# Optimization experiments

Hardware: AMD Instinct MI355X
Metric: run time of the kernel (lower is better)

The kernel has to match this reference:

```python
import jax, jax.numpy as jnp
import numpy as np

B, N = 65536, 128  # batch of point clouds, points per cloud

def setup_inputs() -> dict:
    key = jax.random.key(0)
    k1, k2 = jax.random.split(key)
    x = jax.random.normal(k1, (B, N, 3), dtype=jnp.float32)
    y = jax.random.normal(k2, (B, N, 3), dtype=jnp.float32)
    return {"x": x, "y": y}

def reference(x, y):
    # zero-center both point clouds
    xc = x - x.mean(axis=-2, keepdims=True)
    yc = y - y.mean(axis=-2, keepdims=True)
    # batched 3x3 covariance: C[..., j, k] = sum_i xc[..., i, j] * yc[..., i, k]
    C = jnp.einsum('...ij,...ik->...jk', xc, yc)
    # torch.linalg.svd returns (U, S, Vh); original code names Vh as V and forms R = U @ Vh
    U, _, Vh = jnp.linalg.svd(C)
    R = jnp.einsum('...ij,...jk->...ik', U, Vh)
    x_aligned = jnp.einsum('...ij,...jk->...ik', xc, R)
    # mean square deviation over all batch, point, and coordinate dims
    return jnp.mean((x_aligned - yc) ** 2)
```

## Files before the change

### kernel.cpp

```cpp
#include <hip/hip_runtime.h>
#include <math.h>


#define NPTS 128

__device__ __forceinline__ float xsum(float v, int m) {
    return v + __shfl_xor(v, m);
}

__global__ __launch_bounds__(256, 1) void kabsch_kernel(
        const float* __restrict__ x, const float* __restrict__ y,
        float* __restrict__ out, float scale) {
    const int tid  = threadIdx.x;
    const int lane = tid & 63;
    const int wave = tid >> 6;
    const int g    = lane >> 3;
    const int sub  = lane & 7;
    const int b    = blockIdx.x * 32 + wave * 8 + g;

    const float4* xq = (const float4*)(x + (size_t)b * (NPTS * 3) + sub * 48);
    const float4* yq = (const float4*)(y + (size_t)b * (NPTS * 3) + sub * 48);

    float sx0=0.f,sx1=0.f,sx2=0.f, sy0=0.f,sy1=0.f,sy2=0.f;
    float qx=0.f, qy=0.f;
    float c00=0.f,c01=0.f,c02=0.f,c10=0.f,c11=0.f,c12=0.f,c20=0.f,c21=0.f,c22=0.f;

    #pragma unroll
    for (int h = 0; h < 2; ++h) {
        float4 xv0 = xq[6*h+0], xv1 = xq[6*h+1], xv2 = xq[6*h+2];
        float4 xv3 = xq[6*h+3], xv4 = xq[6*h+4], xv5 = xq[6*h+5];
        float4 yv0 = yq[6*h+0], yv1 = yq[6*h+1], yv2 = yq[6*h+2];
        float4 yv3 = yq[6*h+3], yv4 = yq[6*h+4], yv5 = yq[6*h+5];

        float fx[24], fy[24];
        fx[ 0]=xv0.x; fx[ 1]=xv0.y; fx[ 2]=xv0.z; fx[ 3]=xv0.w;
        fx[ 4]=xv1.x; fx[ 5]=xv1.y; fx[ 6]=xv1.z; fx[ 7]=xv1.w;
        fx[ 8]=xv2.x; fx[ 9]=xv2.y; fx[10]=xv2.z; fx[11]=xv2.w;
        fx[12]=xv3.x; fx[13]=xv3.y; fx[14]=xv3.z; fx[15]=xv3.w;
        fx[16]=xv4.x; fx[17]=xv4.y; fx[18]=xv4.z; fx[19]=xv4.w;
        fx[20]=xv5.x; fx[21]=xv5.y; fx[22]=xv5.z; fx[23]=xv5.w;
        fy[ 0]=yv0.x; fy[ 1]=yv0.y; fy[ 2]=yv0.z; fy[ 3]=yv0.w;
        fy[ 4]=yv1.x; fy[ 5]=yv1.y; fy[ 6]=yv1.z; fy[ 7]=yv1.w;
        fy[ 8]=yv2.x; fy[ 9]=yv2.y; fy[10]=yv2.z; fy[11]=yv2.w;
        fy[12]=yv3.x; fy[13]=yv3.y; fy[14]=yv3.z; fy[15]=yv3.w;
        fy[16]=yv4.x; fy[17]=yv4.y; fy[18]=yv4.z; fy[19]=yv4.w;
        fy[20]=yv5.x; fy[21]=yv5.y; fy[22]=yv5.z; fy[23]=yv5.w;

        #pragma unroll
        for (int p = 0; p < 8; ++p) {
            float px0=fx[3*p], px1=fx[3*p+1], px2=fx[3*p+2];
            float py0=fy[3*p], py1=fy[3*p+1], py2=fy[3*p+2];
            sx0+=px0; sx1+=px1; sx2+=px2;
            sy0+=py0; sy1+=py1; sy2+=py2;
            qx = fmaf(px0,px0,fmaf(px1,px1,fmaf(px2,px2,qx)));
            qy = fmaf(py0,py0,fmaf(py1,py1,fmaf(py2,py2,qy)));
            c00=fmaf(px0,py0,c00); c01=fmaf(px0,py1,c01); c02=fmaf(px0,py2,c02);
            c10=fmaf(px1,py0,c10); c11=fmaf(px1,py1,c11); c12=fmaf(px1,py2,c12);
            c20=fmaf(px2,py0,c20); c21=fmaf(px2,py1,c21); c22=fmaf(px2,py2,c22);
        }
    }

    #pragma unroll
    for (int m = 1; m <= 4; m <<= 1) {
        sx0=xsum(sx0,m); sx1=xsum(sx1,m); sx2=xsum(sx2,m);
        sy0=xsum(sy0,m); sy1=xsum(sy1,m); sy2=xsum(sy2,m);
        qx =xsum(qx ,m); qy =xsum(qy ,m);
        c00=xsum(c00,m); c01=xsum(c01,m); c02=xsum(c02,m);
        c10=xsum(c10,m); c11=xsum(c11,m); c12=xsum(c12,m);
        c20=xsum(c20,m); c21=xsum(c21,m); c22=xsum(c22,m);
    }

    const float invN = 1.0f / (float)NPTS;
    float C00 = c00 - sx0*sy0*invN, C01 = c01 - sx0*sy1*invN, C02 = c02 - sx0*sy2*invN;
    float C10 = c10 - sx1*sy0*invN, C11 = c11 - sx1*sy1*invN, C12 = c12 - sx1*sy2*invN;
    float C20 = c20 - sx2*sy0*invN, C21 = c21 - sx2*sy1*invN, C22 = c22 - sx2*sy2*invN;
    float Sx = qx - (sx0*sx0 + sx1*sx1 + sx2*sx2) * invN;
    float Sy = qy - (sy0*sy0 + sy1*sy1 + sy2*sy2) * invN;

    float a00 = C00*C00 + C10*C10 + C20*C20;
    float a01 = C00*C01 + C10*C11 + C20*C21;
    float a02 = C00*C02 + C10*C12 + C20*C22;
    float a11 = C01*C01 + C11*C11 + C21*C21;
    float a12 = C01*C02 + C11*C12 + C21*C22;
    float a22 = C02*C02 + C12*C12 + C22*C22;

    float q = (a00 + a11 + a22) * (1.0f / 3.0f);
    float b00 = a00 - q, b11 = a11 - q, b22 = a22 - q;
    float p2 = (b00*b00 + b11*b11 + b22*b22
                + 2.0f * (a01*a01 + a02*a02 + a12*a12)) * (1.0f / 6.0f);
    float p = sqrtf(fmaxf(p2, 0.0f));
    float detB = b00 * (b11*b22 - a12*a12)
               - a01 * (a01*b22 - a12*a02)
               + a02 * (a01*a12 - b11*a02);
    float p3 = p * p * p;
    float r = (p3 > 1e-30f) ? (0.5f * detB / p3) : 0.0f;
    r = fminf(1.0f, fmaxf(-1.0f, r));
    float phi = acosf(r) * (1.0f / 3.0f);
    float two_p = 2.0f * p;
    float l1 = q + two_p * cosf(phi);
    float l3 = q + two_p * cosf(phi + 2.0943951023931953f);
    float l2 = 3.0f * q - l1 - l3;
    float nuc = sqrtf(fmaxf(l1, 0.0f)) + sqrtf(fmaxf(l2, 0.0f)) + sqrtf(fmaxf(l3, 0.0f));

    float term = Sx + Sy - 2.0f * nuc;

    term += __shfl_xor(term, 8);
    term += __shfl_xor(term, 16);
    term += __shfl_xor(term, 32);

    __shared__ float wsum[4];
    if (lane == 0) wsum[wave] = term;
    __syncthreads();
    if (tid == 0) {
        float t = (wsum[0] + wsum[1] + wsum[2] + wsum[3]) * scale;
        atomicAdd(out, t);
    }
}

extern "C" void kernel_launch(void* const* d_in, const int* in_sizes, int n_in,
                              void* d_out, int out_size, void* d_ws, size_t ws_size,
                              hipStream_t stream) {
    const float* x = (const float*)d_in[0];
    const float* y = (const float*)d_in[1];
    float* out = (float*)d_out;

    const int B = in_sizes[0] / (NPTS * 3);
    const float scale = 1.0f / ((float)B * (float)NPTS * 3.0f);

    hipMemsetAsync(out, 0, sizeof(float), stream);
    const int blocks = B / 32;
    kabsch_kernel<<<blocks, 256, 0, stream>>>(x, y, out, scale);
}
```

Measured before the change: 258.7 us.

## Stage point clouds through LDS with coalesced direct global-to-LDS loads

Each block now copies its 16 batches of x and y into shared memory using fully coalesced float4 loads, issued as direct global-to-LDS transfers when that builtin is available. Each batch is then processed by 16 lanes instead of 8, and one extra shuffle stage is added to the reduction. The launch-bounds occupancy hint rises from 1 to 3 blocks per CU, and there are twice as many blocks. The goal is to replace the strided per-lane global reads with coalesced ones and get more memory parallelism, at the cost of a block-wide barrier, 48KB of LDS per block, and possible LDS bank conflicts on the 6-float4 stride reads.

```diff
diff --git a/kernel.cpp b/kernel.cpp
--- a/kernel.cpp
+++ b/kernel.cpp
@@ -3,65 +3,91 @@
 
 
 #define NPTS 128
+#define BPB 16
+#define F4B 96
 
 __device__ __forceinline__ float xsum(float v, int m) {
     return v + __shfl_xor(v, m);
 }
 
-__global__ __launch_bounds__(256, 1) void kabsch_kernel(
-        const float* __restrict__ x, const float* __restrict__ y,
+__global__ __launch_bounds__(256, 3) void kabsch_kernel(
+        const float4* __restrict__ x4, const float4* __restrict__ y4,
         float* __restrict__ out, float scale) {
+    __shared__ float4 smem[2 * BPB * F4B];
+
     const int tid  = threadIdx.x;
     const int lane = tid & 63;
     const int wave = tid >> 6;
-    const int g    = lane >> 3;
-    const int sub  = lane & 7;
-    const int b    = blockIdx.x * 32 + wave * 8 + g;
 
-    const float4* xq = (const float4*)(x + (size_t)b * (NPTS * 3) + sub * 48);
-    const float4* yq = (const float4*)(y + (size_t)b * (NPTS * 3) + sub * 48);
+    const size_t blockBase = (size_t)blockIdx.x * (BPB * F4B);
+
+    {
+        const int rpw = (BPB * F4B) / (64 * 4);
+        #pragma unroll
+        for (int j = 0; j < rpw; ++j) {
+            const int idx = (wave * rpw + j) * 64;
+#if defined(__has_builtin)
+#if __has_builtin(__builtin_amdgcn_global_load_lds)
+            __builtin_amdgcn_global_load_lds(
+                (const __attribute__((address_space(1))) void*)(x4 + blockBase + idx + lane),
+                (__attribute__((address_space(3))) void*)(&smem[idx]), 16, 0, 0);
+            __builtin_amdgcn_global_load_lds(
+                (const __attribute__((address_space(1))) void*)(y4 + blockBase + idx + lane),
+                (__attribute__((address_space(3))) void*)(&smem[BPB * F4B + idx]), 16, 0, 0);
+#else
+            smem[idx + lane] = x4[blockBase + idx + lane];
+            smem[BPB * F4B + idx + lane] = y4[blockBase + idx + lane];
+#endif
+#else
+            smem[idx + lane] = x4[blockBase + idx + lane];
+            smem[BPB * F4B + idx + lane] = y4[blockBase + idx + lane];
+#endif
+        }
+    }
+    __syncthreads();
+
+    const int g    = lane >> 4;
+    const int sub  = lane & 15;
+    const int bblk = wave * 4 + g;
+    const float4* xs = &smem[bblk * F4B + sub * 6];
+    const float4* ys = &smem[BPB * F4B + bblk * F4B + sub * 6];
+
+    float4 xv0 = xs[0], xv1 = xs[1], xv2 = xs[2], xv3 = xs[3], xv4 = xs[4], xv5 = xs[5];
+    float4 yv0 = ys[0], yv1 = ys[1], yv2 = ys[2], yv3 = ys[3], yv4 = ys[4], yv5 = ys[5];
+
+    float fx[24], fy[24];
+    fx[ 0]=xv0.x; fx[ 1]=xv0.y; fx[ 2]=xv0.z; fx[ 3]=xv0.w;
+    fx[ 4]=xv1.x; fx[ 5]=xv1.y; fx[ 6]=xv1.z; fx[ 7]=xv1.w;
+    fx[ 8]=xv2.x; fx[ 9]=xv2.y; fx[10]=xv2.z; fx[11]=xv2.w;
+    fx[12]=xv3.x; fx[13]=xv3.y; fx[14]=xv3.z; fx[15]=xv3.w;
+    fx[16]=xv4.x; fx[17]=xv4.y; fx[18]=xv4.z; fx[19]=xv4.w;
+    fx[20]=xv5.x; fx[21]=xv5.y; fx[22]=xv5.z; fx[23]=xv5.w;
+    fy[ 0]=yv0.x; fy[ 1]=yv0.y; fy[ 2]=yv0.z; fy[ 3]=yv0.w;
+    fy[ 4]=yv1.x; fy[ 5]=yv1.y; fy[ 6]=yv1.z; fy[ 7]=yv1.w;
+    fy[ 8]=yv2.x; fy[ 9]=yv2.y; fy[10]=yv2.z; fy[11]=yv2.w;
+    fy[12]=yv3.x; fy[13]=yv3.y; fy[14]=yv3.z; fy[15]=yv3.w;
+    fy[16]=yv4.x; fy[17]=yv4.y; fy[18]=yv4.z; fy[19]=yv4.w;
+    fy[20]=yv5.x; fy[21]=yv5.y; fy[22]=yv5.z; fy[23]=yv5.w;
 
     float sx0=0.f,sx1=0.f,sx2=0.f, sy0=0.f,sy1=0.f,sy2=0.f;
     float qx=0.f, qy=0.f;
     float c00=0.f,c01=0.f,c02=0.f,c10=0.f,c11=0.f,c12=0.f,c20=0.f,c21=0.f,c22=0.f;
 
     #pragma unroll
-    for (int h = 0; h < 2; ++h) {
-        float4 xv0 = xq[6*h+0], xv1 = xq[6*h+1], xv2 = xq[6*h+2];
-        float4 xv3 = xq[6*h+3], xv4 = xq[6*h+4], xv5 = xq[6*h+5];
-        float4 yv0 = yq[6*h+0], yv1 = yq[6*h+1], yv2 = yq[6*h+2];
-        float4 yv3 = yq[6*h+3], yv4 = yq[6*h+4], yv5 = yq[6*h+5];
-
-        float fx[24], fy[24];
-        fx[ 0]=xv0.x; fx[ 1]=xv0.y; fx[ 2]=xv0.z; fx[ 3]=xv0.w;
-        fx[ 4]=xv1.x; fx[ 5]=xv1.y; fx[ 6]=xv1.z; fx[ 7]=xv1.w;
-        fx[ 8]=xv2.x; fx[ 9]=xv2.y; fx[10]=xv2.z; fx[11]=xv2.w;
-        fx[12]=xv3.x; fx[13]=xv3.y; fx[14]=xv3.z; fx[15]=xv3.w;
-        fx[16]=xv4.x; fx[17]=xv4.y; fx[18]=xv4.z; fx[19]=xv4.w;
-        fx[20]=xv5.x; fx[21]=xv5.y; fx[22]=xv5.z; fx[23]=xv5.w;
-        fy[ 0]=yv0.x; fy[ 1]=yv0.y; fy[ 2]=yv0.z; fy[ 3]=yv0.w;
-        fy[ 4]=yv1.x; fy[ 5]=yv1.y; fy[ 6]=yv1.z; fy[ 7]=yv1.w;
-        fy[ 8]=yv2.x; fy[ 9]=yv2.y; fy[10]=yv2.z; fy[11]=yv2.w;
-        fy[12]=yv3.x; fy[13]=yv3.y; fy[14]=yv3.z; fy[15]=yv3.w;
-        fy[16]=yv4.x; fy[17]=yv4.y; fy[18]=yv4.z; fy[19]=yv4.w;
-        fy[20]=yv5.x; fy[21]=yv5.y; fy[22]=yv5.z; fy[23]=yv5.w;
-
-        #pragma unroll
-        for (int p = 0; p < 8; ++p) {
-            float px0=fx[3*p], px1=fx[3*p+1], px2=fx[3*p+2];
-            float py0=fy[3*p], py1=fy[3*p+1], py2=fy[3*p+2];
-            sx0+=px0; sx1+=px1; sx2+=px2;
-            sy0+=py0; sy1+=py1; sy2+=py2;
-            qx = fmaf(px0,px0,fmaf(px1,px1,fmaf(px2,px2,qx)));
-            qy = fmaf(py0,py0,fmaf(py1,py1,fmaf(py2,py2,qy)));
-            c00=fmaf(px0,py0,c00); c01=fmaf(px0,py1,c01); c02=fmaf(px0,py2,c02);
-            c10=fmaf(px1,py0,c10); c11=fmaf(px1,py1,c11); c12=fmaf(px1,py2,c12);
-            c20=fmaf(px2,py0,c20); c21=fmaf(px2,py1,c21); c22=fmaf(px2,py2,c22);
-        }
+    for (int p = 0; p < 8; ++p) {
+        float px0=fx[3*p], px1=fx[3*p+1], px2=fx[3*p+2];
+        float py0=fy[3*p], py1=fy[3*p+1], py2=fy[3*p+2];
+        sx0+=px0; sx1+=px1; sx2+=px2;
+        sy0+=py0; sy1+=py1; sy2+=py2;
+        qx = fmaf(px0,px0,fmaf(px1,px1,fmaf(px2,px2,qx)));
+        qy = fmaf(py0,py0,fmaf(py1,py1,fmaf(py2,py2,qy)));
+        c00=fmaf(px0,py0,c00); c01=fmaf(px0,py1,c01); c02=fmaf(px0,py2,c02);
+        c10=fmaf(px1,py0,c10); c11=fmaf(px1,py1,c11); c12=fmaf(px1,py2,c12);
+        c20=fmaf(px2,py0,c20); c21=fmaf(px2,py1,c21); c22=fmaf(px2,py2,c22);
     }
 
     #pragma unroll
-    for (int m = 1; m <= 4; m <<= 1) {
+    for (int m = 1; m <= 8; m <<= 1) {
         sx0=xsum(sx0,m); sx1=xsum(sx1,m); sx2=xsum(sx2,m);
         sy0=xsum(sy0,m); sy1=xsum(sy1,m); sy2=xsum(sy2,m);
         qx =xsum(qx ,m); qy =xsum(qy ,m);
@@ -104,7 +130,6 @@
 
     float term = Sx + Sy - 2.0f * nuc;
 
-    term += __shfl_xor(term, 8);
     term += __shfl_xor(term, 16);
     term += __shfl_xor(term, 32);
 
@@ -120,14 +145,14 @@
 extern "C" void kernel_launch(void* const* d_in, const int* in_sizes, int n_in,
                               void* d_out, int out_size, void* d_ws, size_t ws_size,
                               hipStream_t stream) {
-    const float* x = (const float*)d_in[0];
-    const float* y = (const float*)d_in[1];
+    const float4* x4 = (const float4*)d_in[0];
+    const float4* y4 = (const float4*)d_in[1];
     float* out = (float*)d_out;
 
     const int B = in_sizes[0] / (NPTS * 3);
     const float scale = 1.0f / ((float)B * (float)NPTS * 3.0f);
 
     hipMemsetAsync(out, 0, sizeof(float), stream);
-    const int blocks = B / 32;
-    kabsch_kernel<<<blocks, 256, 0, stream>>>(x, y, out, scale);
+    const int blocks = B / BPB;
+    kabsch_kernel<<<blocks, 256, 0, stream>>>(x4, y4, out, scale);
 }
```

Result: faster. 215.3 us (-16.8%).

## Persistent waves with double-buffered global-to-LDS async tile prefetch

Applied to the files above, without the earlier changes.

Replaces one-block-per-32-clouds launch with a fixed persistent grid where each wave loops over tiles of two point clouds. Tiles are prefetched into per-wave LDS double buffers using direct global-to-LDS loads, overlapping the next tile's fetch with the current tile's covariance and eigenvalue math. Each cloud is now reduced across 32 lanes instead of 8, which adds shuffle steps and duplicates the closed-form eigen solve across more lanes. Occupancy is limited by the fixed grid and the LDS use.

```diff
diff --git a/kernel.cpp b/kernel.cpp
--- a/kernel.cpp
+++ b/kernel.cpp
@@ -3,51 +3,82 @@
 
 
 #define NPTS 128
+#define WPB 4
+#define BLOCKS 512
+#define TOTAL_WAVES (BLOCKS * WPB)
+#define TILE_F4 192
+#define BUF_F4 (2 * TILE_F4)
 
 __device__ __forceinline__ float xsum(float v, int m) {
     return v + __shfl_xor(v, m);
 }
 
-__global__ __launch_bounds__(256, 1) void kabsch_kernel(
-        const float* __restrict__ x, const float* __restrict__ y,
-        float* __restrict__ out, float scale) {
+__device__ __forceinline__ void stage_tile(const float4* __restrict__ x4,
+                                           const float4* __restrict__ y4,
+                                           size_t tile, float4* buf, int lane) {
+    const size_t base = tile * TILE_F4;
+    #pragma unroll
+    for (int r = 0; r < 3; ++r) {
+        __builtin_amdgcn_global_load_lds(
+            (const __attribute__((address_space(1))) void*)(x4 + base + r * 64 + lane),
+            (__attribute__((address_space(3))) void*)(buf + r * 64), 16, 0, 0);
+        __builtin_amdgcn_global_load_lds(
+            (const __attribute__((address_space(1))) void*)(y4 + base + r * 64 + lane),
+            (__attribute__((address_space(3))) void*)(buf + TILE_F4 + r * 64), 16, 0, 0);
+    }
+}
+
+__global__ __launch_bounds__(256, 2) void kabsch_kernel(
+        const float4* __restrict__ x4, const float4* __restrict__ y4,
+        float* __restrict__ out, float scale, int tilesPerWave) {
+    __shared__ float4 smem[WPB][2][BUF_F4];
+    __shared__ float wsum[WPB];
+
     const int tid  = threadIdx.x;
     const int lane = tid & 63;
     const int wave = tid >> 6;
-    const int g    = lane >> 3;
-    const int sub  = lane & 7;
-    const int b    = blockIdx.x * 32 + wave * 8 + g;
+    const int w    = blockIdx.x * WPB + wave;
 
-    const float4* xq = (const float4*)(x + (size_t)b * (NPTS * 3) + sub * 48);
-    const float4* yq = (const float4*)(y + (size_t)b * (NPTS * 3) + sub * 48);
+    float4* buf0 = &smem[wave][0][0];
+    float4* buf1 = &smem[wave][1][0];
 
-    float sx0=0.f,sx1=0.f,sx2=0.f, sy0=0.f,sy1=0.f,sy2=0.f;
-    float qx=0.f, qy=0.f;
-    float c00=0.f,c01=0.f,c02=0.f,c10=0.f,c11=0.f,c12=0.f,c20=0.f,c21=0.f,c22=0.f;
+    stage_tile(x4, y4, (size_t)w, buf0, lane);
 
-    #pragma unroll
-    for (int h = 0; h < 2; ++h) {
-        float4 xv0 = xq[6*h+0], xv1 = xq[6*h+1], xv2 = xq[6*h+2];
-        float4 xv3 = xq[6*h+3], xv4 = xq[6*h+4], xv5 = xq[6*h+5];
-        float4 yv0 = yq[6*h+0], yv1 = yq[6*h+1], yv2 = yq[6*h+2];
-        float4 yv3 = yq[6*h+3], yv4 = yq[6*h+4], yv5 = yq[6*h+5];
+    const int g   = lane >> 5;
+    const int sub = lane & 31;
+    const float invN = 1.0f / (float)NPTS;
 
-        float fx[24], fy[24];
-        fx[ 0]=xv0.x; fx[ 1]=xv0.y; fx[ 2]=xv0.z; fx[ 3]=xv0.w;
-        fx[ 4]=xv1.x; fx[ 5]=xv1.y; fx[ 6]=xv1.z; fx[ 7]=xv1.w;
-        fx[ 8]=xv2.x; fx[ 9]=xv2.y; fx[10]=xv2.z; fx[11]=xv2.w;
-        fx[12]=xv3.x; fx[13]=xv3.y; fx[14]=xv3.z; fx[15]=xv3.w;
-        fx[16]=xv4.x; fx[17]=xv4.y; fx[18]=xv4.z; fx[19]=xv4.w;
-        fx[20]=xv5.x; fx[21]=xv5.y; fx[22]=xv5.z; fx[23]=xv5.w;
-        fy[ 0]=yv0.x; fy[ 1]=yv0.y; fy[ 2]=yv0.z; fy[ 3]=yv0.w;
-        fy[ 4]=yv1.x; fy[ 5]=yv1.y; fy[ 6]=yv1.z; fy[ 7]=yv1.w;
-        fy[ 8]=yv2.x; fy[ 9]=yv2.y; fy[10]=yv2.z; fy[11]=yv2.w;
-        fy[12]=yv3.x; fy[13]=yv3.y; fy[14]=yv3.z; fy[15]=yv3.w;
-        fy[16]=yv4.x; fy[17]=yv4.y; fy[18]=yv4.z; fy[19]=yv4.w;
-        fy[20]=yv5.x; fy[21]=yv5.y; fy[22]=yv5.z; fy[23]=yv5.w;
+    float wave_acc = 0.f;
+
+    for (int t = 0; t < tilesPerWave; ++t) {
+        float4* cur = (t & 1) ? buf1 : buf0;
+        float4* nxt = (t & 1) ? buf0 : buf1;
+
+        asm volatile("s_waitcnt vmcnt(0)" ::: "memory");
+
+        const float4* xs = cur + g * 96 + sub * 3;
+        const float4* ys = cur + TILE_F4 + g * 96 + sub * 3;
+        float4 xv0 = xs[0], xv1 = xs[1], xv2 = xs[2];
+        float4 yv0 = ys[0], yv1 = ys[1], yv2 = ys[2];
+
+        if (t + 1 < tilesPerWave)
+            stage_tile(x4, y4, (size_t)w + (size_t)(t + 1) * TOTAL_WAVES, nxt, lane);
+
+        float fx[12], fy[12];
+        fx[0]=xv0.x; fx[1]=xv0.y; fx[2]=xv0.z; fx[3]=xv0.w;
+        fx[4]=xv1.x; fx[5]=xv1.y; fx[6]=xv1.z; fx[7]=xv1.w;
+        fx[8]=xv2.x; fx[9]=xv2.y; fx[10]=xv2.z; fx[11]=xv2.w;
+        fy[0]=yv0.x; fy[1]=yv0.y; fy[2]=yv0.z; fy[3]=yv0.w;
+        fy[4]=yv1.x; fy[5]=yv1.y; fy[6]=yv1.z; fy[7]=yv1.w;
+        fy[8]=yv2.x; fy[9]=yv2.y; fy[10]=yv2.z; fy[11]=yv2.w;
+
+        float sx0=0.f,sx1=0.f,sx2=0.f, sy0=0.f,sy1=0.f,sy2=0.f;
+        float qx=0.f, qy=0.f;
+        float c00=0.f,c01=0.f,c02=0.f,c10=0.f,c11=0.f,c12=0.f,
+              c20=0.f,c21=0.f,c22=0.f;
 
         #pragma unroll
-        for (int p = 0; p < 8; ++p) {
+        for (int p = 0; p < 4; ++p) {
             float px0=fx[3*p], px1=fx[3*p+1], px2=fx[3*p+2];
             float py0=fy[3*p], py1=fy[3*p+1], py2=fy[3*p+2];
             sx0+=px0; sx1+=px1; sx2+=px2;
@@ -58,76 +89,74 @@
             c10=fmaf(px1,py0,c10); c11=fmaf(px1,py1,c11); c12=fmaf(px1,py2,c12);
             c20=fmaf(px2,py0,c20); c21=fmaf(px2,py1,c21); c22=fmaf(px2,py2,c22);
         }
+
+        #pragma unroll
+        for (int m = 1; m <= 16; m <<= 1) {
+            sx0=xsum(sx0,m); sx1=xsum(sx1,m); sx2=xsum(sx2,m);
+            sy0=xsum(sy0,m); sy1=xsum(sy1,m); sy2=xsum(sy2,m);
+            qx =xsum(qx ,m); qy =xsum(qy ,m);
+            c00=xsum(c00,m); c01=xsum(c01,m); c02=xsum(c02,m);
+            c10=xsum(c10,m); c11=xsum(c11,m); c12=xsum(c12,m);
+            c20=xsum(c20,m); c21=xsum(c21,m); c22=xsum(c22,m);
+        }
+
+        float C00 = c00 - sx0*sy0*invN, C01 = c01 - sx0*sy1*invN, C02 = c02 - sx0*sy2*invN;
+        float C10 = c10 - sx1*sy0*invN, C11 = c11 - sx1*sy1*invN, C12 = c12 - sx1*sy2*invN;
+        float C20 = c20 - sx2*sy0*invN, C21 = c21 - sx2*sy1*invN, C22 = c22 - sx2*sy2*invN;
+        float Sx = qx - (sx0*sx0 + sx1*sx1 + sx2*sx2) * invN;
+        float Sy = qy - (sy0*sy0 + sy1*sy1 + sy2*sy2) * invN;
+
+        float a00 = C00*C00 + C10*C10 + C20*C20;
+        float a01 = C00*C01 + C10*C11 + C20*C21;
+        float a02 = C00*C02 + C10*C12 + C20*C22;
+        float a11 = C01*C01 + C11*C11 + C21*C21;
+        float a12 = C01*C02 + C11*C12 + C21*C22;
+        float a22 = C02*C02 + C12*C12 + C22*C22;
+
+        float q = (a00 + a11 + a22) * (1.0f / 3.0f);
+        float b00 = a00 - q, b11 = a11 - q, b22 = a22 - q;
+        float p2 = (b00*b00 + b11*b11 + b22*b22
+                    + 2.0f * (a01*a01 + a02*a02 + a12*a12)) * (1.0f / 6.0f);
+        float p = sqrtf(fmaxf(p2, 0.0f));
+        float detB = b00 * (b11*b22 - a12*a12)
+                   - a01 * (a01*b22 - a12*a02)
+                   + a02 * (a01*a12 - b11*a02);
+        float p3 = p * p * p;
+        float r = (p3 > 1e-30f) ? (0.5f * detB / p3) : 0.0f;
+        r = fminf(1.0f, fmaxf(-1.0f, r));
+        float phi = acosf(r) * (1.0f / 3.0f);
+        float two_p = 2.0f * p;
+        float l1 = q + two_p * cosf(phi);
+        float l3 = q + two_p * cosf(phi + 2.0943951023931953f);
+        float l2 = 3.0f * q - l1 - l3;
+        float nuc = sqrtf(fmaxf(l1, 0.0f)) + sqrtf(fmaxf(l2, 0.0f))
+                  + sqrtf(fmaxf(l3, 0.0f));
+
+        float term = Sx + Sy - 2.0f * nuc;
+        term += __shfl_xor(term, 32);
+        wave_acc += term;
     }
 
-    #pragma unroll
-    for (int m = 1; m <= 4; m <<= 1) {
-        sx0=xsum(sx0,m); sx1=xsum(sx1,m); sx2=xsum(sx2,m);
-        sy0=xsum(sy0,m); sy1=xsum(sy1,m); sy2=xsum(sy2,m);
-        qx =xsum(qx ,m); qy =xsum(qy ,m);
-        c00=xsum(c00,m); c01=xsum(c01,m); c02=xsum(c02,m);
-        c10=xsum(c10,m); c11=xsum(c11,m); c12=xsum(c12,m);
-        c20=xsum(c20,m); c21=xsum(c21,m); c22=xsum(c22,m);
-    }
-
-    const float invN = 1.0f / (float)NPTS;
-    float C00 = c00 - sx0*sy0*invN, C01 = c01 - sx0*sy1*invN, C02 = c02 - sx0*sy2*invN;
-    float C10 = c10 - sx1*sy0*invN, C11 = c11 - sx1*sy1*invN, C12 = c12 - sx1*sy2*invN;
-    float C20 = c20 - sx2*sy0*invN, C21 = c21 - sx2*sy1*invN, C22 = c22 - sx2*sy2*invN;
-    float Sx = qx - (sx0*sx0 + sx1*sx1 + sx2*sx2) * invN;
-    float Sy = qy - (sy0*sy0 + sy1*sy1 + sy2*sy2) * invN;
-
-    float a00 = C00*C00 + C10*C10 + C20*C20;
-    float a01 = C00*C01 + C10*C11 + C20*C21;
-    float a02 = C00*C02 + C10*C12 + C20*C22;
-    float a11 = C01*C01 + C11*C11 + C21*C21;
-    float a12 = C01*C02 + C11*C12 + C21*C22;
-    float a22 = C02*C02 + C12*C12 + C22*C22;
-
-    float q = (a00 + a11 + a22) * (1.0f / 3.0f);
-    float b00 = a00 - q, b11 = a11 - q, b22 = a22 - q;
-    float p2 = (b00*b00 + b11*b11 + b22*b22
-                + 2.0f * (a01*a01 + a02*a02 + a12*a12)) * (1.0f / 6.0f);
-    float p = sqrtf(fmaxf(p2, 0.0f));
-    float detB = b00 * (b11*b22 - a12*a12)
-               - a01 * (a01*b22 - a12*a02)
-               + a02 * (a01*a12 - b11*a02);
-    float p3 = p * p * p;
-    float r = (p3 > 1e-30f) ? (0.5f * detB / p3) : 0.0f;
-    r = fminf(1.0f, fmaxf(-1.0f, r));
-    float phi = acosf(r) * (1.0f / 3.0f);
-    float two_p = 2.0f * p;
-    float l1 = q + two_p * cosf(phi);
-    float l3 = q + two_p * cosf(phi + 2.0943951023931953f);
-    float l2 = 3.0f * q - l1 - l3;
-    float nuc = sqrtf(fmaxf(l1, 0.0f)) + sqrtf(fmaxf(l2, 0.0f)) + sqrtf(fmaxf(l3, 0.0f));
-
-    float term = Sx + Sy - 2.0f * nuc;
-
-    term += __shfl_xor(term, 8);
-    term += __shfl_xor(term, 16);
-    term += __shfl_xor(term, 32);
-
-    __shared__ float wsum[4];
-    if (lane == 0) wsum[wave] = term;
+    if (lane == 0) wsum[wave] = wave_acc;
     __syncthreads();
     if (tid == 0) {
-        float t = (wsum[0] + wsum[1] + wsum[2] + wsum[3]) * scale;
-        atomicAdd(out, t);
+        float tsum = (wsum[0] + wsum[1] + wsum[2] + wsum[3]) * scale;
+        atomicAdd(out, tsum);
     }
 }
 
 extern "C" void kernel_launch(void* const* d_in, const int* in_sizes, int n_in,
                               void* d_out, int out_size, void* d_ws, size_t ws_size,
                               hipStream_t stream) {
-    const float* x = (const float*)d_in[0];
-    const float* y = (const float*)d_in[1];
+    const float4* x4 = (const float4*)d_in[0];
+    const float4* y4 = (const float4*)d_in[1];
     float* out = (float*)d_out;
 
     const int B = in_sizes[0] / (NPTS * 3);
+    const int totalTiles = B / 2;
+    const int tilesPerWave = totalTiles / TOTAL_WAVES;
     const float scale = 1.0f / ((float)B * (float)NPTS * 3.0f);
 
     hipMemsetAsync(out, 0, sizeof(float), stream);
-    const int blocks = B / 32;
-    kabsch_kernel<<<blocks, 256, 0, stream>>>(x, y, out, scale);
+    kabsch_kernel<<<BLOCKS, WPB * 64, 0, stream>>>(x4, y4, out, scale, tilesPerWave);
 }
```

Result: faster. 216.1 us (-16.5%).
